# Performance work log

Measured on AMD Instinct MI355X. Metric: run time of the kernel, lower is better.

The kernel has to match this reference:

```python
import jax, jax.numpy as jnp
import numpy as np

B, C, H, W = 128, 2048, 14, 14
K = 112          # num_concepts
NUM_CLASSES = 200


def setup_inputs() -> dict:
    key = jax.random.key(0)
    ks = jax.random.split(key, 8)
    x = jax.random.normal(ks[0], (B, C, H, W), dtype=jnp.float32)
    concepts = jax.random.normal(ks[1], (K, C), dtype=jnp.float32)
    modulation = jax.random.normal(ks[2], (1, C), dtype=jnp.float32)
    background = jax.random.normal(ks[3], (1, C), dtype=jnp.float32)
    # concept_fc: Linear(C, 1)
    w_cfc = jax.random.normal(ks[4], (1, C), dtype=jnp.float32) / np.sqrt(C)
    b_cfc = jnp.zeros((1,), dtype=jnp.float32)
    # label_fc: Linear(C*K, num_classes)
    w_lfc = jax.random.normal(ks[5], (NUM_CLASSES, C * K), dtype=jnp.float32) / np.sqrt(C * K)
    b_lfc = jnp.zeros((NUM_CLASSES,), dtype=jnp.float32)
    return {"x": x, "concepts": concepts, "modulation": modulation,
            "background": background, "w_cfc": w_cfc, "b_cfc": b_cfc,
            "w_lfc": w_lfc, "b_lfc": b_lfc}


def reference(x, concepts, modulation, background, w_cfc, b_cfc, w_lfc, b_lfc):
    b, c, h, w = x.shape
    n = h * w
    x_flat = x.reshape(b, c, n).transpose(0, 2, 1)          # [b, n, c]
    cpts_wbg = jnp.concatenate([concepts, background], 0)   # [k+1, c]

    # cdist p=2 via ||a||^2 + ||x||^2 - 2 a.x
    a_sq = jnp.sum(cpts_wbg * cpts_wbg, -1)                 # [k+1]
    x_sq = jnp.sum(x_flat * x_flat, -1)                     # [b, n]
    dots = jnp.einsum('kc,bnc->bkn', cpts_wbg, x_flat)      # [b, k+1, n]
    d2 = a_sq[None, :, None] + x_sq[:, None, :] - 2.0 * dots
    dists = jnp.sqrt(jnp.maximum(d2, 0.0))                  # [b, k+1, n]

    attn = jax.nn.softmax(-dists, axis=1)                   # softmax over concepts
    cpt_score_maps = attn.reshape(b, -1, h, w)              # [b, k+1, h, w]

    cpt_reprs = jnp.einsum('bkn,bnc->bkc', attn[:, :-1, :], x_flat)  # [b, k, c]
    cpt_logits = jax.nn.sigmoid(
        jnp.einsum('bkc,oc->bko', cpt_reprs, w_cfc) + b_cfc).squeeze(-1)  # [b, k]

    g = cpt_logits[..., None]                               # [b, k, 1]
    cpts_mixed = g * concepts[None] + (1.0 - g) * modulation[None]  # [b, k, c]
    label_logits = cpts_mixed.reshape(b, -1) @ w_lfc.T + b_lfc      # [b, classes]

    return cpt_score_maps, cpt_logits, label_logits
```

## Files before the change

### kernel.cpp

```cpp
#include <hip/hip_runtime.h>
#include <hip/hip_bf16.h>
#include <math.h>

#define B 128
#define C 2048
#define N 196
#define K 112
#define KB 113
#define MROWS 128
#define XWROW 113
#define NCLS 200
#define CKC (C * K)
#define NT 13
#define MAIN_BLKS 416
#define PQ_BLKS 5600

#define OUT1_OFF 2834944
#define OUT2_OFF 2849280

typedef __attribute__((ext_vector_type(8))) short bf16x8;
typedef __attribute__((ext_vector_type(4))) float f32x4;

__device__ inline unsigned cvtpk(float a, float b) {
    union { __hip_bfloat162 h; unsigned u; } c;
    c.h.x = __float2bfloat16(a);
    c.h.y = __float2bfloat16(b);
    return c.u;
}
__device__ inline const float* row_src(int row, const float* concepts,
                                       const float* background, const float* wcfc) {
    if (row < K) return concepts + (size_t)row * C;
    if (row == K) return background;
    if (row == XWROW) return wcfc;
    return nullptr;
}
__device__ __forceinline__ void gl16(const void* g, void* l) {
    __builtin_amdgcn_global_load_lds(
        (const __attribute__((address_space(1))) unsigned*)g,
        (__attribute__((address_space(3))) unsigned*)l, 16, 0, 0);
}

__global__ __launch_bounds__(256)
void asq_kernel(const float* __restrict__ concepts, const float* __restrict__ background,
                const float* __restrict__ wcfc, float* __restrict__ asq) {
    const int row = blockIdx.x;
    const int tid = threadIdx.x;
    const float* src = row_src(row, concepts, background, wcfc);
    float local = 0.f;
    if (src) for (int i = tid; i < C; i += 256) { float v = src[i]; local += v * v; }
    for (int off = 32; off; off >>= 1) local += __shfl_down(local, off);
    __shared__ float red[4];
    if ((tid & 63) == 0) red[tid >> 6] = local;
    __syncthreads();
    if (tid == 0) asq[row] = red[0] + red[1] + red[2] + red[3];
}

__global__ __launch_bounds__(64)
void pack_kernel(const float* __restrict__ concepts, const float* __restrict__ background,
                 const float* __restrict__ wcfc, unsigned short* __restrict__ Afrag) {
    const int f = blockIdx.x;
    const int it = blockIdx.y;
    const int l = threadIdx.x;
    const int row = 16 * f + (l & 15);
    const int kb = 32 * it + 8 * (l >> 4);
    const float* src = row_src(row, concepts, background, wcfc);
    unsigned o[4] = {0u, 0u, 0u, 0u};
    if (src) {
        const float4 f0 = *reinterpret_cast<const float4*>(src + kb);
        const float4 f1 = *reinterpret_cast<const float4*>(src + kb + 4);
        o[0] = cvtpk(f0.x, f0.y); o[1] = cvtpk(f0.z, f0.w);
        o[2] = cvtpk(f1.x, f1.y); o[3] = cvtpk(f1.z, f1.w);
    }
    *reinterpret_cast<uint4*>(Afrag + (((size_t)it * 8 + f) * 64 + l) * 8) =
        make_uint4(o[0], o[1], o[2], o[3]);
}

__global__ __launch_bounds__(256, 2)
void fused_kernel(const float* __restrict__ x,
                  const unsigned short* __restrict__ Afrag,
                  const float* __restrict__ asq_g,
                  float* __restrict__ out0,
                  float* __restrict__ lpart,
                  const float* __restrict__ wlfc,
                  const float* __restrict__ concepts,
                  const float* __restrict__ modulation,
                  float* __restrict__ Rm, float* __restrict__ Qs) {
    __shared__ __align__(16) char smem[65536];
    const int tid = threadIdx.x;
    const int lane = tid & 63;
    const int w = tid >> 6;
    const int blkid = blockIdx.x;

    if (blkid < MAIN_BLKS) {
        const int gw = blkid * 4 + w;
        const int b = gw / NT;
        const int nt = gw - b * NT;
        const int n0 = nt * 16;
        const int lo = lane & 15, hi = lane >> 4;

        char* Abase = smem;
        char* Xw = smem + 32768 + w * 8192;

        const char* agl = (const char*)Afrag + w * 1024 + lane * 16;
        const int xr = lane >> 2, xc = lane & 3;
        const bool bad = (nt == NT - 1) && (xc != 0);
        const float* xlane = bad ? x
            : x + (size_t)b * C * N + (size_t)xr * N + (n0 + xc * 4);
        const char* xgl = (const char*)xlane;

        f32x4 acc[8];
#pragma unroll
        for (int f = 0; f < 8; ++f) acc[f] = (f32x4){0.f, 0.f, 0.f, 0.f};
        float xs = 0.f;

#define STAGE(SBUF) do {                                                        \
        gl16(agl,        Abase + (SBUF) * 8192 + 0 * 4096 + w * 1024);          \
        gl16(agl + 4096, Abase + (SBUF) * 8192 + 1 * 4096 + w * 1024);          \
        gl16(xgl,                  Xw + (SBUF) * 2048);                         \
        gl16(xgl + 16 * N * 4,     Xw + (SBUF) * 2048 + 1024);                  \
        agl += 8192; xgl += (size_t)32 * N * 4;                                 \
    } while (0)

#define PIPE_WAIT(NSTR) do {                                                    \
        asm volatile("s_waitcnt vmcnt(" NSTR ")" ::: "memory");                 \
        __builtin_amdgcn_sched_barrier(0);                                      \
        __builtin_amdgcn_s_barrier();                                           \
        asm volatile("" ::: "memory");                                          \
        __builtin_amdgcn_sched_barrier(0);                                      \
    } while (0)

#define CONS(BUF) do {                                                          \
        bf16x8 af[8];                                                           \
        _Pragma("unroll")                                                       \
        for (int f = 0; f < 8; ++f)                                             \
            af[f] = *reinterpret_cast<const bf16x8*>(                           \
                Abase + (BUF) * 8192 + f * 1024 + (lane << 4));                 \
        float xv[8];                                                            \
        _Pragma("unroll")                                                       \
        for (int j = 0; j < 8; ++j)                                             \
            xv[j] = *reinterpret_cast<const float*>(                            \
                Xw + (BUF) * 2048 + ((hi * 8 + j) << 6) + (lo << 2));           \
        union { unsigned u[4]; bf16x8 v; } bu;                                  \
        _Pragma("unroll")                                                       \
        for (int p = 0; p < 4; ++p) bu.u[p] = cvtpk(xv[2 * p], xv[2 * p + 1]); \
        _Pragma("unroll")                                                       \
        for (int j = 0; j < 8; ++j) xs += xv[j] * xv[j];                        \
        _Pragma("unroll")                                                       \
        for (int f = 0; f < 8; ++f)                                             \
            acc[f] = __builtin_amdgcn_mfma_f32_16x16x32_bf16(                   \
                af[f], bu.v, acc[f], 0, 0, 0);                                  \
    } while (0)

        STAGE(0); STAGE(1);
        for (int trip = 0; trip < 15; ++trip) {
            STAGE(2); PIPE_WAIT("8"); CONS(0);
            STAGE(3); PIPE_WAIT("8"); CONS(1);
            STAGE(0); PIPE_WAIT("8"); CONS(2);
            STAGE(1); PIPE_WAIT("8"); CONS(3);
        }
        STAGE(2); PIPE_WAIT("8"); CONS(0);
        STAGE(3); PIPE_WAIT("8"); CONS(1);
        PIPE_WAIT("4"); CONS(2);
        PIPE_WAIT("0"); CONS(3);

        float xsq = xs + __shfl_xor(xs, 16);
        xsq += __shfl_xor(xsq, 32);
        const float xw = __shfl(acc[7][1], lo);
        const int colg = n0 + lo;
        const bool colv = colg < N;

        float m = -3.4e38f;
#pragma unroll
        for (int f = 0; f < 8; ++f)
#pragma unroll
            for (int rr = 0; rr < 4; ++rr) {
                const int r = 16 * f + 4 * hi + rr;
                const bool valid = (f < 7) | ((hi == 0) & (rr == 0));
                if (valid) {
                    const float d2 = asq_g[r] + xsq - 2.f * acc[f][rr];
                    const float L = -sqrtf(fmaxf(d2, 0.f));
                    acc[f][rr] = L;
                    m = fmaxf(m, L);
                }
            }
        float M = fmaxf(m, __shfl_xor(m, 16));
        M = fmaxf(M, __shfl_xor(M, 32));
        float s = 0.f;
#pragma unroll
        for (int f = 0; f < 8; ++f)
#pragma unroll
            for (int rr = 0; rr < 4; ++rr) {
                const bool valid = (f < 7) | ((hi == 0) & (rr == 0));
                const float e = valid ? __expf(acc[f][rr] - M) : 0.f;
                acc[f][rr] = e;
                s += e;
            }
        float S = s + __shfl_xor(s, 16);
        S += __shfl_xor(S, 32);
        const float invS = 1.f / S;

        float* o0 = out0 + (size_t)b * KB * N + colg;
#pragma unroll
        for (int f = 0; f < 8; ++f)
#pragma unroll
            for (int rr = 0; rr < 4; ++rr) {
                const int r = 16 * f + 4 * hi + rr;
                const bool valid = (f < 7) | ((hi == 0) & (rr == 0));
                if (valid && colv) o0[(size_t)r * N] = acc[f][rr] * invS;
            }
#pragma unroll
        for (int f = 0; f < 7; ++f)
#pragma unroll
            for (int rr = 0; rr < 4; ++rr) {
                float pv = colv ? acc[f][rr] * invS * xw : 0.f;
                pv += __shfl_xor(pv, 1);
                pv += __shfl_xor(pv, 2);
                pv += __shfl_xor(pv, 4);
                pv += __shfl_xor(pv, 8);
                if (lo == 0)
                    lpart[((size_t)b * NT + nt) * K + 16 * f + 4 * hi + rr] = pv;
            }
    } else {
        const int wid = (blkid - MAIN_BLKS) * 4 + w;
        const int o = wid / K;
        const int k = wid % K;
        const float4* wp = reinterpret_cast<const float4*>(wlfc + (size_t)o * CKC + (size_t)k * C);
        const float4* cp = reinterpret_cast<const float4*>(concepts + (size_t)k * C);
        const float4* mp = reinterpret_cast<const float4*>(modulation);
        float s1 = 0.f, s2 = 0.f;
#pragma unroll
        for (int it = 0; it < 8; ++it) {
            const int idx = it * 64 + lane;
            const float4 w4 = wp[idx];
            const float4 c4 = cp[idx];
            const float4 m4 = mp[idx];
            s1 += w4.x * c4.x + w4.y * c4.y + w4.z * c4.z + w4.w * c4.w;
            s2 += w4.x * m4.x + w4.y * m4.y + w4.z * m4.z + w4.w * m4.w;
        }
        for (int off = 32; off; off >>= 1) {
            s1 += __shfl_down(s1, off);
            s2 += __shfl_down(s2, off);
        }
        if (lane == 0) { Rm[wid] = s1 - s2; Qs[wid] = s2; }
    }
}

__global__ __launch_bounds__(256)
void final_kernel(const float* __restrict__ lpart, const float* __restrict__ bcfc,
                  const float* __restrict__ Rm, const float* __restrict__ Qs,
                  const float* __restrict__ blfc,
                  float* __restrict__ out1, float* __restrict__ out2) {
    const int b = blockIdx.x;
    const int tid = threadIdx.x;
    __shared__ float g_s[K];
    if (tid < K) {
        const float* lp = lpart + (size_t)b * NT * K + tid;
        float v = bcfc[0];
#pragma unroll
        for (int t = 0; t < NT; ++t) v += lp[(size_t)t * K];
        const float g = 1.f / (1.f + __expf(-v));
        out1[b * K + tid] = g;
        g_s[tid] = g;
    }
    __syncthreads();
    if (tid < NCLS) {
        float acc = blfc[tid];
        const float* rp = Rm + (size_t)tid * K;
        const float* qp = Qs + (size_t)tid * K;
        for (int k = 0; k < K; ++k) acc = fmaf(g_s[k], rp[k], acc) + qp[k];
        out2[b * NCLS + tid] = acc;
    }
}

extern "C" void kernel_launch(void* const* d_in, const int* in_sizes, int n_in,
                              void* d_out, int out_size, void* d_ws, size_t ws_size,
                              hipStream_t stream) {
    const float* x          = (const float*)d_in[0];
    const float* concepts   = (const float*)d_in[1];
    const float* modulation = (const float*)d_in[2];
    const float* background = (const float*)d_in[3];
    const float* wcfc       = (const float*)d_in[4];
    const float* bcfc       = (const float*)d_in[5];
    const float* wlfc       = (const float*)d_in[6];
    const float* blfc       = (const float*)d_in[7];

    float* out  = (float*)d_out;
    float* out0 = out;
    float* out1 = out + OUT1_OFF;
    float* out2 = out + OUT2_OFF;

    float* ws    = (float*)d_ws;
    float* asq   = ws;
    float* lpart = asq + MROWS;
    float* Rm    = lpart + (size_t)B * NT * K;
    float* Qs    = Rm + NCLS * K;
    unsigned short* Afrag = (unsigned short*)(Qs + NCLS * K);

    asq_kernel<<<MROWS, 256, 0, stream>>>(concepts, background, wcfc, asq);
    pack_kernel<<<dim3(8, 64), 64, 0, stream>>>(concepts, background, wcfc, Afrag);
    fused_kernel<<<MAIN_BLKS + PQ_BLKS, 256, 0, stream>>>(
        x, Afrag, asq, out0, lpart, wlfc, concepts, modulation, Rm, Qs);
    final_kernel<<<B, 256, 0, stream>>>(lpart, bcfc, Rm, Qs, blfc, out1, out2);
}
```

Measured before the change: 112.0 us.

## Use single-wave blocks with 32-column tiles and triple-buffered A staging

Restructures the fused kernel to launch 64-thread blocks, each handling a 32-column slice of one batch with two MFMA accumulators per A fragment. The A-fragment loads are reused across both column halves, and block-wide barriers disappear because each block is a single wave. The pipeline becomes three-stage and the PQ section loops over four dot products per wave. The change cuts barrier cost and raises reuse of A. In exchange, each wave now loads the full A tile itself, because it can no longer be shared across four waves, and it holds more registers for the doubled accumulators.

Result: slower. 129.1 us (+15.2%).

```diff
diff --git a/kernel.cpp b/kernel.cpp
--- a/kernel.cpp
+++ b/kernel.cpp
@@ -11,8 +11,8 @@
 #define XWROW 113
 #define NCLS 200
 #define CKC (C * K)
-#define NT 13
-#define MAIN_BLKS 416
+#define NT 7
+#define MAIN_BLKS 896
 #define PQ_BLKS 5600
 
 #define OUT1_OFF 2834944
@@ -75,7 +75,7 @@
         make_uint4(o[0], o[1], o[2], o[3]);
 }
 
-__global__ __launch_bounds__(256, 2)
+__global__ __launch_bounds__(64)
 void fused_kernel(const float* __restrict__ x,
                   const unsigned short* __restrict__ Afrag,
                   const float* __restrict__ asq_g,
@@ -85,91 +85,101 @@
                   const float* __restrict__ concepts,
                   const float* __restrict__ modulation,
                   float* __restrict__ Rm, float* __restrict__ Qs) {
-    __shared__ __align__(16) char smem[65536];
-    const int tid = threadIdx.x;
-    const int lane = tid & 63;
-    const int w = tid >> 6;
+    __shared__ __align__(16) char smem[36864];
+    const int lane = threadIdx.x;
     const int blkid = blockIdx.x;
 
     if (blkid < MAIN_BLKS) {
-        const int gw = blkid * 4 + w;
-        const int b = gw / NT;
-        const int nt = gw - b * NT;
-        const int n0 = nt * 16;
+        const int b = blkid / NT;
+        const int nt = blkid - b * NT;
+        const int n0 = nt * 32;
         const int lo = lane & 15, hi = lane >> 4;
 
         char* Abase = smem;
-        char* Xw = smem + 32768 + w * 8192;
-
-        const char* agl = (const char*)Afrag + w * 1024 + lane * 16;
-        const int xr = lane >> 2, xc = lane & 3;
-        const bool bad = (nt == NT - 1) && (xc != 0);
-        const float* xlane = bad ? x
-            : x + (size_t)b * C * N + (size_t)xr * N + (n0 + xc * 4);
-        const char* xgl = (const char*)xlane;
-
-        f32x4 acc[8];
-#pragma unroll
-        for (int f = 0; f < 8; ++f) acc[f] = (f32x4){0.f, 0.f, 0.f, 0.f};
-        float xs = 0.f;
-
-#define STAGE(SBUF) do {                                                        \
-        gl16(agl,        Abase + (SBUF) * 8192 + 0 * 4096 + w * 1024);          \
-        gl16(agl + 4096, Abase + (SBUF) * 8192 + 1 * 4096 + w * 1024);          \
-        gl16(xgl,                  Xw + (SBUF) * 2048);                         \
-        gl16(xgl + 16 * N * 4,     Xw + (SBUF) * 2048 + 1024);                  \
+        char* Xbase = smem + 24576;
+
+        const char* agl = (const char*)Afrag + lane * 16;
+        const int segb_raw = n0 * 4 + (lane & 7) * 16;
+        const int segb = segb_raw < (N - 4) * 4 ? segb_raw : (N - 4) * 4;
+        const char* xgl = (const char*)x
+            + ((size_t)b * C + (lane >> 3)) * N * 4 + segb;
+
+        f32x4 acc[8][2];
+#pragma unroll
+        for (int f = 0; f < 8; ++f) {
+            acc[f][0] = (f32x4){0.f, 0.f, 0.f, 0.f};
+            acc[f][1] = (f32x4){0.f, 0.f, 0.f, 0.f};
+        }
+        float xs0 = 0.f, xs1 = 0.f;
+
+#define STAGE(BUF) do {                                                         \
+        _Pragma("unroll")                                                       \
+        for (int i_ = 0; i_ < 8; ++i_)                                          \
+            gl16(agl + i_ * 1024, Abase + (BUF) * 8192 + i_ * 1024);            \
+        _Pragma("unroll")                                                       \
+        for (int i_ = 0; i_ < 4; ++i_)                                          \
+            gl16(xgl + (size_t)i_ * 8 * N * 4, Xbase + (BUF) * 4096 + i_ * 1024);\
         agl += 8192; xgl += (size_t)32 * N * 4;                                 \
     } while (0)
 
 #define PIPE_WAIT(NSTR) do {                                                    \
         asm volatile("s_waitcnt vmcnt(" NSTR ")" ::: "memory");                 \
         __builtin_amdgcn_sched_barrier(0);                                      \
-        __builtin_amdgcn_s_barrier();                                           \
-        asm volatile("" ::: "memory");                                          \
-        __builtin_amdgcn_sched_barrier(0);                                      \
     } while (0)
 
 #define CONS(BUF) do {                                                          \
         bf16x8 af[8];                                                           \
         _Pragma("unroll")                                                       \
-        for (int f = 0; f < 8; ++f)                                             \
-            af[f] = *reinterpret_cast<const bf16x8*>(                           \
-                Abase + (BUF) * 8192 + f * 1024 + (lane << 4));                 \
-        float xv[8];                                                            \
-        _Pragma("unroll")                                                       \
-        for (int j = 0; j < 8; ++j)                                             \
-            xv[j] = *reinterpret_cast<const float*>(                            \
-                Xw + (BUF) * 2048 + ((hi * 8 + j) << 6) + (lo << 2));           \
-        union { unsigned u[4]; bf16x8 v; } bu;                                  \
-        _Pragma("unroll")                                                       \
-        for (int p = 0; p < 4; ++p) bu.u[p] = cvtpk(xv[2 * p], xv[2 * p + 1]); \
-        _Pragma("unroll")                                                       \
-        for (int j = 0; j < 8; ++j) xs += xv[j] * xv[j];                        \
-        _Pragma("unroll")                                                       \
-        for (int f = 0; f < 8; ++f)                                             \
-            acc[f] = __builtin_amdgcn_mfma_f32_16x16x32_bf16(                   \
-                af[f], bu.v, acc[f], 0, 0, 0);                                  \
+        for (int f_ = 0; f_ < 8; ++f_)                                          \
+            af[f_] = *reinterpret_cast<const bf16x8*>(                          \
+                Abase + (BUF) * 8192 + f_ * 1024 + (lane << 4));                \
+        float xv0[8], xv1[8];                                                   \
+        _Pragma("unroll")                                                       \
+        for (int j_ = 0; j_ < 8; ++j_) {                                        \
+            xv0[j_] = *reinterpret_cast<const float*>(                          \
+                Xbase + (BUF) * 4096 + ((hi * 8 + j_) << 7) + (lo << 2));       \
+            xv1[j_] = *reinterpret_cast<const float*>(                          \
+                Xbase + (BUF) * 4096 + ((hi * 8 + j_) << 7) + ((16 + lo) << 2));\
+        }                                                                       \
+        union { unsigned u[4]; bf16x8 v; } b0_, b1_;                            \
+        _Pragma("unroll")                                                       \
+        for (int p_ = 0; p_ < 4; ++p_) {                                        \
+            b0_.u[p_] = cvtpk(xv0[2 * p_], xv0[2 * p_ + 1]);                    \
+            b1_.u[p_] = cvtpk(xv1[2 * p_], xv1[2 * p_ + 1]);                    \
+        }                                                                       \
+        _Pragma("unroll")                                                       \
+        for (int j_ = 0; j_ < 8; ++j_) {                                        \
+            xs0 += xv0[j_] * xv0[j_];                                           \
+            xs1 += xv1[j_] * xv1[j_];                                           \
+        }                                                                       \
+        _Pragma("unroll")                                                       \
+        for (int f_ = 0; f_ < 8; ++f_) {                                        \
+            acc[f_][0] = __builtin_amdgcn_mfma_f32_16x16x32_bf16(               \
+                af[f_], b0_.v, acc[f_][0], 0, 0, 0);                            \
+            acc[f_][1] = __builtin_amdgcn_mfma_f32_16x16x32_bf16(               \
+                af[f_], b1_.v, acc[f_][1], 0, 0, 0);                            \
+        }                                                                       \
     } while (0)
 
         STAGE(0); STAGE(1);
-        for (int trip = 0; trip < 15; ++trip) {
-            STAGE(2); PIPE_WAIT("8"); CONS(0);
-            STAGE(3); PIPE_WAIT("8"); CONS(1);
-            STAGE(0); PIPE_WAIT("8"); CONS(2);
-            STAGE(1); PIPE_WAIT("8"); CONS(3);
+        for (int tp = 0; tp < 20; ++tp) {
+            PIPE_WAIT("12"); STAGE(2); CONS(0);
+            PIPE_WAIT("12"); STAGE(0); CONS(1);
+            PIPE_WAIT("12"); STAGE(1); CONS(2);
         }
-        STAGE(2); PIPE_WAIT("8"); CONS(0);
-        STAGE(3); PIPE_WAIT("8"); CONS(1);
-        PIPE_WAIT("4"); CONS(2);
-        PIPE_WAIT("0"); CONS(3);
-
-        float xsq = xs + __shfl_xor(xs, 16);
-        xsq += __shfl_xor(xsq, 32);
-        const float xw = __shfl(acc[7][1], lo);
-        const int colg = n0 + lo;
-        const bool colv = colg < N;
-
-        float m = -3.4e38f;
+        PIPE_WAIT("12"); STAGE(2); CONS(0);
+        PIPE_WAIT("12"); STAGE(0); CONS(1);
+        PIPE_WAIT("12"); CONS(2);
+        PIPE_WAIT("0");  CONS(0);
+
+        float xsq0 = xs0 + __shfl_xor(xs0, 16); xsq0 += __shfl_xor(xsq0, 32);
+        float xsq1 = xs1 + __shfl_xor(xs1, 16); xsq1 += __shfl_xor(xsq1, 32);
+        const float xw0 = __shfl(acc[7][0][1], lo);
+        const float xw1 = __shfl(acc[7][1][1], lo);
+        const bool cv0 = (n0 + lo) < N;
+        const bool cv1 = (n0 + 16 + lo) < N;
+
+        float m0 = -3.4e38f, m1 = -3.4e38f;
 #pragma unroll
         for (int f = 0; f < 8; ++f)
 #pragma unroll
@@ -177,42 +187,46 @@
                 const int r = 16 * f + 4 * hi + rr;
                 const bool valid = (f < 7) | ((hi == 0) & (rr == 0));
                 if (valid) {
-                    const float d2 = asq_g[r] + xsq - 2.f * acc[f][rr];
-                    const float L = -sqrtf(fmaxf(d2, 0.f));
-                    acc[f][rr] = L;
-                    m = fmaxf(m, L);
+                    const float aq = asq_g[r];
+                    float L0 = -sqrtf(fmaxf(aq + xsq0 - 2.f * acc[f][0][rr], 0.f));
+                    float L1 = -sqrtf(fmaxf(aq + xsq1 - 2.f * acc[f][1][rr], 0.f));
+                    acc[f][0][rr] = L0; acc[f][1][rr] = L1;
+                    m0 = fmaxf(m0, L0); m1 = fmaxf(m1, L1);
                 }
             }
-        float M = fmaxf(m, __shfl_xor(m, 16));
-        M = fmaxf(M, __shfl_xor(M, 32));
-        float s = 0.f;
+        float M0 = fmaxf(m0, __shfl_xor(m0, 16)); M0 = fmaxf(M0, __shfl_xor(M0, 32));
+        float M1 = fmaxf(m1, __shfl_xor(m1, 16)); M1 = fmaxf(M1, __shfl_xor(M1, 32));
+        float s0 = 0.f, s1 = 0.f;
 #pragma unroll
         for (int f = 0; f < 8; ++f)
 #pragma unroll
             for (int rr = 0; rr < 4; ++rr) {
                 const bool valid = (f < 7) | ((hi == 0) & (rr == 0));
-                const float e = valid ? __expf(acc[f][rr] - M) : 0.f;
-                acc[f][rr] = e;
-                s += e;
-            }
-        float S = s + __shfl_xor(s, 16);
-        S += __shfl_xor(S, 32);
-        const float invS = 1.f / S;
-
-        float* o0 = out0 + (size_t)b * KB * N + colg;
+                const float e0 = valid ? __expf(acc[f][0][rr] - M0) : 0.f;
+                const float e1 = valid ? __expf(acc[f][1][rr] - M1) : 0.f;
+                acc[f][0][rr] = e0; acc[f][1][rr] = e1;
+                s0 += e0; s1 += e1;
+            }
+        float S0 = s0 + __shfl_xor(s0, 16); S0 += __shfl_xor(S0, 32);
+        float S1 = s1 + __shfl_xor(s1, 16); S1 += __shfl_xor(S1, 32);
+        const float iv0 = 1.f / S0, iv1 = 1.f / S1;
+
+        float* o0 = out0 + (size_t)b * KB * N + n0 + lo;
 #pragma unroll
         for (int f = 0; f < 8; ++f)
 #pragma unroll
             for (int rr = 0; rr < 4; ++rr) {
                 const int r = 16 * f + 4 * hi + rr;
                 const bool valid = (f < 7) | ((hi == 0) & (rr == 0));
-                if (valid && colv) o0[(size_t)r * N] = acc[f][rr] * invS;
+                if (valid && cv0) o0[(size_t)r * N] = acc[f][0][rr] * iv0;
+                if (valid && cv1) o0[(size_t)r * N + 16] = acc[f][1][rr] * iv1;
             }
 #pragma unroll
         for (int f = 0; f < 7; ++f)
 #pragma unroll
             for (int rr = 0; rr < 4; ++rr) {
-                float pv = colv ? acc[f][rr] * invS * xw : 0.f;
+                float pv = (cv0 ? acc[f][0][rr] * iv0 * xw0 : 0.f)
+                         + (cv1 ? acc[f][1][rr] * iv1 * xw1 : 0.f);
                 pv += __shfl_xor(pv, 1);
                 pv += __shfl_xor(pv, 2);
                 pv += __shfl_xor(pv, 4);
@@ -221,27 +235,31 @@
                     lpart[((size_t)b * NT + nt) * K + 16 * f + 4 * hi + rr] = pv;
             }
     } else {
-        const int wid = (blkid - MAIN_BLKS) * 4 + w;
-        const int o = wid / K;
-        const int k = wid % K;
-        const float4* wp = reinterpret_cast<const float4*>(wlfc + (size_t)o * CKC + (size_t)k * C);
-        const float4* cp = reinterpret_cast<const float4*>(concepts + (size_t)k * C);
-        const float4* mp = reinterpret_cast<const float4*>(modulation);
-        float s1 = 0.f, s2 = 0.f;
-#pragma unroll
-        for (int it = 0; it < 8; ++it) {
-            const int idx = it * 64 + lane;
-            const float4 w4 = wp[idx];
-            const float4 c4 = cp[idx];
-            const float4 m4 = mp[idx];
-            s1 += w4.x * c4.x + w4.y * c4.y + w4.z * c4.z + w4.w * c4.w;
-            s2 += w4.x * m4.x + w4.y * m4.y + w4.z * m4.z + w4.w * m4.w;
+        const int wb = (blkid - MAIN_BLKS) * 4;
+#pragma unroll
+        for (int q = 0; q < 4; ++q) {
+            const int wid = wb + q;
+            const int o = wid / K;
+            const int k = wid % K;
+            const float4* wp = reinterpret_cast<const float4*>(wlfc + (size_t)o * CKC + (size_t)k * C);
+            const float4* cp = reinterpret_cast<const float4*>(concepts + (size_t)k * C);
+            const float4* mp = reinterpret_cast<const float4*>(modulation);
+            float s1 = 0.f, s2 = 0.f;
+#pragma unroll
+            for (int it = 0; it < 8; ++it) {
+                const int idx = it * 64 + lane;
+                const float4 w4 = wp[idx];
+                const float4 c4 = cp[idx];
+                const float4 m4 = mp[idx];
+                s1 += w4.x * c4.x + w4.y * c4.y + w4.z * c4.z + w4.w * c4.w;
+                s2 += w4.x * m4.x + w4.y * m4.y + w4.z * m4.z + w4.w * m4.w;
+            }
+            for (int off = 32; off; off >>= 1) {
+                s1 += __shfl_down(s1, off);
+                s2 += __shfl_down(s2, off);
+            }
+            if (lane == 0) { Rm[wid] = s1 - s2; Qs[wid] = s2; }
         }
-        for (int off = 32; off; off >>= 1) {
-            s1 += __shfl_down(s1, off);
-            s2 += __shfl_down(s2, off);
-        }
-        if (lane == 0) { Rm[wid] = s1 - s2; Qs[wid] = s2; }
     }
 }
 
@@ -298,7 +316,7 @@
 
     asq_kernel<<<MROWS, 256, 0, stream>>>(concepts, background, wcfc, asq);
     pack_kernel<<<dim3(8, 64), 64, 0, stream>>>(concepts, background, wcfc, Afrag);
-    fused_kernel<<<MAIN_BLKS + PQ_BLKS, 256, 0, stream>>>(
+    fused_kernel<<<MAIN_BLKS + PQ_BLKS, 64, 0, stream>>>(
         x, Afrag, asq, out0, lpart, wlfc, concepts, modulation, Rm, Qs);
     final_kernel<<<B, 256, 0, stream>>>(lpart, bcfc, Rm, Qs, blfc, out1, out2);
 }
```

## Process one whole image per 512-thread block with an LDS-transposed bf16 X tile

Applied to the files above, without the earlier changes.

The main GEMM is restructured so each block owns a full image (all 196 spatial columns) and each of its 8 waves owns one 16-row concept fragment. X chunks are loaded contiguously into LDS, converted to bf16 and transposed in a separate pass, then reused across 13 column tiles, so each A fragment is loaded once per image instead of once per 16-column tile. The softmax max and sum now need cross-wave reductions through LDS, and the per-tile lpart partials disappear. The pipeline is shallower, with a double-buffered A, a single-buffered X and several barriers per step, and the grid shrinks to 128 main blocks, which may leave the GPU underfilled.

Result: slower. 121.3 us (+8.2%).

```diff
diff --git a/kernel.cpp b/kernel.cpp
--- a/kernel.cpp
+++ b/kernel.cpp
@@ -11,9 +11,10 @@
 #define XWROW 113
 #define NCLS 200
 #define CKC (C * K)
-#define NT 13
-#define MAIN_BLKS 416
-#define PQ_BLKS 5600
+#define MAIN_BLKS 128
+#define PQ_BLKS 700
+#define XSTEP 25088
+#define IMGB (C * N * 4)
 
 #define OUT1_OFF 2834944
 #define OUT2_OFF 2849280
@@ -38,6 +39,11 @@
     __builtin_amdgcn_global_load_lds(
         (const __attribute__((address_space(1))) unsigned*)g,
         (__attribute__((address_space(3))) unsigned*)l, 16, 0, 0);
+}
+__device__ __forceinline__ void gl4(const void* g, void* l) {
+    __builtin_amdgcn_global_load_lds(
+        (const __attribute__((address_space(1))) unsigned*)g,
+        (__attribute__((address_space(3))) unsigned*)l, 4, 0, 0);
 }
 
 __global__ __launch_bounds__(256)
@@ -59,10 +65,10 @@
 void pack_kernel(const float* __restrict__ concepts, const float* __restrict__ background,
                  const float* __restrict__ wcfc, unsigned short* __restrict__ Afrag) {
     const int f = blockIdx.x;
-    const int it = blockIdx.y;
+    const int kwg = blockIdx.y;
     const int l = threadIdx.x;
     const int row = 16 * f + (l & 15);
-    const int kb = 32 * it + 8 * (l >> 4);
+    const int kb = 32 * kwg + 8 * (l >> 4);
     const float* src = row_src(row, concepts, background, wcfc);
     unsigned o[4] = {0u, 0u, 0u, 0u};
     if (src) {
@@ -71,11 +77,11 @@
         o[0] = cvtpk(f0.x, f0.y); o[1] = cvtpk(f0.z, f0.w);
         o[2] = cvtpk(f1.x, f1.y); o[3] = cvtpk(f1.z, f1.w);
     }
-    *reinterpret_cast<uint4*>(Afrag + (((size_t)it * 8 + f) * 64 + l) * 8) =
+    *reinterpret_cast<uint4*>(Afrag + (((size_t)kwg * 8 + f) * 64 + l) * 8) =
         make_uint4(o[0], o[1], o[2], o[3]);
 }
 
-__global__ __launch_bounds__(256, 2)
+__global__ __launch_bounds__(512)
 void fused_kernel(const float* __restrict__ x,
                   const unsigned short* __restrict__ Afrag,
                   const float* __restrict__ asq_g,
@@ -85,163 +91,236 @@
                   const float* __restrict__ concepts,
                   const float* __restrict__ modulation,
                   float* __restrict__ Rm, float* __restrict__ Qs) {
-    __shared__ __align__(16) char smem[65536];
+    __shared__ __align__(16) char smem[61952];
     const int tid = threadIdx.x;
     const int lane = tid & 63;
     const int w = tid >> 6;
     const int blkid = blockIdx.x;
 
     if (blkid < MAIN_BLKS) {
-        const int gw = blkid * 4 + w;
-        const int b = gw / NT;
-        const int nt = gw - b * NT;
-        const int n0 = nt * 16;
+        const int b = blkid;
+        float* Xf = (float*)smem;
+        char* Ab0 = smem + 25600;
+        unsigned short* XT = (unsigned short*)(smem + 41984);
+        float* xsqL = (float*)(smem + 58624);
+        float* pmw = (float*)smem;
+        float* xwL = (float*)(smem + 8192);
+
         const int lo = lane & 15, hi = lane >> 4;
-
-        char* Abase = smem;
-        char* Xw = smem + 32768 + w * 8192;
-
-        const char* agl = (const char*)Afrag + w * 1024 + lane * 16;
-        const int xr = lane >> 2, xc = lane & 3;
-        const bool bad = (nt == NT - 1) && (xc != 0);
-        const float* xlane = bad ? x
-            : x + (size_t)b * C * N + (size_t)xr * N + (n0 + xc * 4);
-        const char* xgl = (const char*)xlane;
-
-        f32x4 acc[8];
-#pragma unroll
-        for (int f = 0; f < 8; ++f) acc[f] = (f32x4){0.f, 0.f, 0.f, 0.f};
+        const char* xim = (const char*)x + (size_t)b * IMGB;
+        const char* Ag = (const char*)Afrag;
+
+        const bool act = tid < 416;
+        const int h = (act && tid >= 208) ? 1 : 0;
+        const int cc = act ? (tid - 208 * h) : 0;
+
+        f32x4 acc[13];
+#pragma unroll
+        for (int ct = 0; ct < 13; ++ct) acc[ct] = (f32x4){0.f, 0.f, 0.f, 0.f};
         float xs = 0.f;
 
-#define STAGE(SBUF) do {                                                        \
-        gl16(agl,        Abase + (SBUF) * 8192 + 0 * 4096 + w * 1024);          \
-        gl16(agl + 4096, Abase + (SBUF) * 8192 + 1 * 4096 + w * 1024);          \
-        gl16(xgl,                  Xw + (SBUF) * 2048);                         \
-        gl16(xgl + 16 * N * 4,     Xw + (SBUF) * 2048 + 1024);                  \
-        agl += 8192; xgl += (size_t)32 * N * 4;                                 \
-    } while (0)
-
-#define PIPE_WAIT(NSTR) do {                                                    \
-        asm volatile("s_waitcnt vmcnt(" NSTR ")" ::: "memory");                 \
+#define ISSUE_X(JJ) do {                                                        \
+        const char* sx_ = xim + (size_t)(JJ) * XSTEP;                           \
+        gl16(sx_ + (3 * w + 0) * 1024 + lane * 16, smem + (3 * w + 0) * 1024);  \
+        gl16(sx_ + (3 * w + 1) * 1024 + lane * 16, smem + (3 * w + 1) * 1024);  \
+        gl16(sx_ + (3 * w + 2) * 1024 + lane * 16, smem + (3 * w + 2) * 1024);  \
+        if (w < 2) gl4(sx_ + 24576 + w * 256 + lane * 4,                        \
+                       smem + 24576 + w * 256);                                 \
+    } while (0)
+
+#define ISSUE_A(JJ) do {                                                        \
+        gl16(Ag + (size_t)(JJ) * 8192 + w * 1024 + lane * 16,                   \
+             Ab0 + ((JJ) & 1) * 8192 + w * 1024);                               \
+    } while (0)
+
+#define VM0() do {                                                              \
+        asm volatile("s_waitcnt vmcnt(0)" ::: "memory");                        \
         __builtin_amdgcn_sched_barrier(0);                                      \
+    } while (0)
+
+#define LBAR() do {                                                             \
+        asm volatile("s_waitcnt lgkmcnt(0)" ::: "memory");                      \
         __builtin_amdgcn_s_barrier();                                           \
-        asm volatile("" ::: "memory");                                          \
         __builtin_amdgcn_sched_barrier(0);                                      \
     } while (0)
 
-#define CONS(BUF) do {                                                          \
-        bf16x8 af[8];                                                           \
+#define CONVERT() do {                                                          \
+        if (act) {                                                              \
+            const float* xp_ = Xf + (16 * h) * 196 + cc;                        \
+            float v_[16];                                                       \
+            _Pragma("unroll")                                                   \
+            for (int q_ = 0; q_ < 16; ++q_) v_[q_] = xp_[q_ * 196];             \
+            _Pragma("unroll")                                                   \
+            for (int q_ = 0; q_ < 16; ++q_) xs += v_[q_] * v_[q_];              \
+            unsigned u_[8];                                                     \
+            _Pragma("unroll")                                                   \
+            for (int p_ = 0; p_ < 8; ++p_)                                      \
+                u_[p_] = cvtpk(v_[2 * p_], v_[2 * p_ + 1]);                     \
+            unsigned short* xt_ = XT + cc * 40 + h * 16;                        \
+            *reinterpret_cast<uint4*>(xt_) = make_uint4(u_[0], u_[1], u_[2], u_[3]); \
+            *reinterpret_cast<uint4*>(xt_ + 8) = make_uint4(u_[4], u_[5], u_[6], u_[7]); \
+        }                                                                       \
+    } while (0)
+
+#define MFMA_STEP(JJ) do {                                                      \
+        const char* Ab_ = Ab0 + ((JJ) & 1) * 8192;                              \
+        const bf16x8 afr_ = *reinterpret_cast<const bf16x8*>(                   \
+            Ab_ + ((w * 64 + lane) << 4));                                      \
         _Pragma("unroll")                                                       \
-        for (int f = 0; f < 8; ++f)                                             \
-            af[f] = *reinterpret_cast<const bf16x8*>(                           \
-                Abase + (BUF) * 8192 + f * 1024 + (lane << 4));                 \
-        float xv[8];                                                            \
-        _Pragma("unroll")                                                       \
-        for (int j = 0; j < 8; ++j)                                             \
-            xv[j] = *reinterpret_cast<const float*>(                            \
-                Xw + (BUF) * 2048 + ((hi * 8 + j) << 6) + (lo << 2));           \
-        union { unsigned u[4]; bf16x8 v; } bu;                                  \
-        _Pragma("unroll")                                                       \
-        for (int p = 0; p < 4; ++p) bu.u[p] = cvtpk(xv[2 * p], xv[2 * p + 1]); \
-        _Pragma("unroll")                                                       \
-        for (int j = 0; j < 8; ++j) xs += xv[j] * xv[j];                        \
-        _Pragma("unroll")                                                       \
-        for (int f = 0; f < 8; ++f)                                             \
-            acc[f] = __builtin_amdgcn_mfma_f32_16x16x32_bf16(                   \
-                af[f], bu.v, acc[f], 0, 0, 0);                                  \
-    } while (0)
-
-        STAGE(0); STAGE(1);
-        for (int trip = 0; trip < 15; ++trip) {
-            STAGE(2); PIPE_WAIT("8"); CONS(0);
-            STAGE(3); PIPE_WAIT("8"); CONS(1);
-            STAGE(0); PIPE_WAIT("8"); CONS(2);
-            STAGE(1); PIPE_WAIT("8"); CONS(3);
-        }
-        STAGE(2); PIPE_WAIT("8"); CONS(0);
-        STAGE(3); PIPE_WAIT("8"); CONS(1);
-        PIPE_WAIT("4"); CONS(2);
-        PIPE_WAIT("0"); CONS(3);
-
-        float xsq = xs + __shfl_xor(xs, 16);
-        xsq += __shfl_xor(xsq, 32);
-        const float xw = __shfl(acc[7][1], lo);
-        const int colg = n0 + lo;
-        const bool colv = colg < N;
-
-        float m = -3.4e38f;
-#pragma unroll
-        for (int f = 0; f < 8; ++f)
+        for (int ct_ = 0; ct_ < 13; ++ct_) {                                    \
+            const bf16x8 bfr_ = *reinterpret_cast<const bf16x8*>(               \
+                (const char*)XT + (ct_ * 16 + lo) * 80 + hi * 16);              \
+            acc[ct_] = __builtin_amdgcn_mfma_f32_16x16x32_bf16(                 \
+                afr_, bfr_, acc[ct_], 0, 0, 0);                                 \
+        }                                                                       \
+    } while (0)
+
+        ISSUE_X(0); ISSUE_A(0);
+#pragma unroll 1
+        for (int j = 0; j < 63; ++j) {
+            VM0(); LBAR();
+            CONVERT();
+            LBAR();
+            ISSUE_X(j + 1);
+            MFMA_STEP(j);
+            ISSUE_A(j + 1);
+        }
+        VM0(); LBAR(); CONVERT(); LBAR(); MFMA_STEP(63);
+
+        __syncthreads();
+        if (act) xsqL[h * 208 + cc] = xs;
+        if (w == 7 && hi == 0) {
+#pragma unroll
+            for (int ct = 0; ct < 13; ++ct) xwL[ct * 16 + lo] = acc[ct][1];
+        }
+        __syncthreads();
+
+        float xq[13];
+#pragma unroll
+        for (int ct = 0; ct < 13; ++ct) {
+            const int c = ct * 16 + lo;
+            xq[ct] = xsqL[c] + xsqL[208 + c];
+        }
+        float aq[4];
+#pragma unroll
+        for (int rr = 0; rr < 4; ++rr) aq[rr] = asq_g[16 * w + 4 * hi + rr];
+        const bool v4 = (w < 7);
+
+        float mct[13];
+#pragma unroll
+        for (int ct = 0; ct < 13; ++ct) {
 #pragma unroll
             for (int rr = 0; rr < 4; ++rr) {
-                const int r = 16 * f + 4 * hi + rr;
-                const bool valid = (f < 7) | ((hi == 0) & (rr == 0));
-                if (valid) {
-                    const float d2 = asq_g[r] + xsq - 2.f * acc[f][rr];
-                    const float L = -sqrtf(fmaxf(d2, 0.f));
-                    acc[f][rr] = L;
-                    m = fmaxf(m, L);
+                const float d2 = aq[rr] + xq[ct] - 2.f * acc[ct][rr];
+                acc[ct][rr] = -sqrtf(fmaxf(d2, 0.f));
+            }
+            float mv = -3.4e38f;
+            if (v4) mv = fmaxf(fmaxf(acc[ct][0], acc[ct][1]),
+                               fmaxf(acc[ct][2], acc[ct][3]));
+            else if (hi == 0) mv = acc[ct][0];
+            mv = fmaxf(mv, __shfl_xor(mv, 16));
+            mv = fmaxf(mv, __shfl_xor(mv, 32));
+            mct[ct] = mv;
+        }
+        if (hi == 0) {
+#pragma unroll
+            for (int ct = 0; ct < 13; ++ct) pmw[w * 208 + ct * 16 + lo] = mct[ct];
+        }
+        __syncthreads();
+        float Mct[13];
+#pragma unroll
+        for (int ct = 0; ct < 13; ++ct) {
+            float mm = -3.4e38f;
+#pragma unroll
+            for (int ww = 0; ww < 8; ++ww)
+                mm = fmaxf(mm, pmw[ww * 208 + ct * 16 + lo]);
+            Mct[ct] = mm;
+        }
+        __syncthreads();
+        float sct[13];
+#pragma unroll
+        for (int ct = 0; ct < 13; ++ct) {
+            float ss = 0.f;
+#pragma unroll
+            for (int rr = 0; rr < 4; ++rr) {
+                const bool valid = v4 || (hi == 0 && rr == 0);
+                const float e = valid ? __expf(acc[ct][rr] - Mct[ct]) : 0.f;
+                acc[ct][rr] = e;
+                ss += e;
+            }
+            ss += __shfl_xor(ss, 16);
+            ss += __shfl_xor(ss, 32);
+            sct[ct] = ss;
+        }
+        if (hi == 0) {
+#pragma unroll
+            for (int ct = 0; ct < 13; ++ct) pmw[w * 208 + ct * 16 + lo] = sct[ct];
+        }
+        __syncthreads();
+        float inv[13];
+#pragma unroll
+        for (int ct = 0; ct < 13; ++ct) {
+            float SS = 0.f;
+#pragma unroll
+            for (int ww = 0; ww < 8; ++ww) SS += pmw[ww * 208 + ct * 16 + lo];
+            inv[ct] = 1.f / SS;
+        }
+
+        float* o0 = out0 + (size_t)b * KB * N;
+#pragma unroll
+        for (int ct = 0; ct < 13; ++ct) {
+            const int c = ct * 16 + lo;
+            const bool cv = c < N;
+#pragma unroll
+            for (int rr = 0; rr < 4; ++rr) {
+                const int r = 16 * w + 4 * hi + rr;
+                const bool valid = v4 || (hi == 0 && rr == 0);
+                if (valid && cv) o0[(size_t)r * N + c] = acc[ct][rr] * inv[ct];
+            }
+        }
+        if (v4) {
+#pragma unroll
+            for (int rr = 0; rr < 4; ++rr) {
+                float pv = 0.f;
+#pragma unroll
+                for (int ct = 0; ct < 13; ++ct) {
+                    const int c = ct * 16 + lo;
+                    const float term = acc[ct][rr] * inv[ct] * xwL[c];
+                    pv += (c < N) ? term : 0.f;
                 }
-            }
-        float M = fmaxf(m, __shfl_xor(m, 16));
-        M = fmaxf(M, __shfl_xor(M, 32));
-        float s = 0.f;
-#pragma unroll
-        for (int f = 0; f < 8; ++f)
-#pragma unroll
-            for (int rr = 0; rr < 4; ++rr) {
-                const bool valid = (f < 7) | ((hi == 0) & (rr == 0));
-                const float e = valid ? __expf(acc[f][rr] - M) : 0.f;
-                acc[f][rr] = e;
-                s += e;
-            }
-        float S = s + __shfl_xor(s, 16);
-        S += __shfl_xor(S, 32);
-        const float invS = 1.f / S;
-
-        float* o0 = out0 + (size_t)b * KB * N + colg;
-#pragma unroll
-        for (int f = 0; f < 8; ++f)
-#pragma unroll
-            for (int rr = 0; rr < 4; ++rr) {
-                const int r = 16 * f + 4 * hi + rr;
-                const bool valid = (f < 7) | ((hi == 0) & (rr == 0));
-                if (valid && colv) o0[(size_t)r * N] = acc[f][rr] * invS;
-            }
-#pragma unroll
-        for (int f = 0; f < 7; ++f)
-#pragma unroll
-            for (int rr = 0; rr < 4; ++rr) {
-                float pv = colv ? acc[f][rr] * invS * xw : 0.f;
                 pv += __shfl_xor(pv, 1);
                 pv += __shfl_xor(pv, 2);
                 pv += __shfl_xor(pv, 4);
                 pv += __shfl_xor(pv, 8);
-                if (lo == 0)
-                    lpart[((size_t)b * NT + nt) * K + 16 * f + 4 * hi + rr] = pv;
-            }
+                if (lo == 0) lpart[(size_t)b * K + 16 * w + 4 * hi + rr] = pv;
+            }
+        }
     } else {
-        const int wid = (blkid - MAIN_BLKS) * 4 + w;
-        const int o = wid / K;
-        const int k = wid % K;
-        const float4* wp = reinterpret_cast<const float4*>(wlfc + (size_t)o * CKC + (size_t)k * C);
-        const float4* cp = reinterpret_cast<const float4*>(concepts + (size_t)k * C);
-        const float4* mp = reinterpret_cast<const float4*>(modulation);
-        float s1 = 0.f, s2 = 0.f;
-#pragma unroll
-        for (int it = 0; it < 8; ++it) {
-            const int idx = it * 64 + lane;
-            const float4 w4 = wp[idx];
-            const float4 c4 = cp[idx];
-            const float4 m4 = mp[idx];
-            s1 += w4.x * c4.x + w4.y * c4.y + w4.z * c4.z + w4.w * c4.w;
-            s2 += w4.x * m4.x + w4.y * m4.y + w4.z * m4.z + w4.w * m4.w;
-        }
-        for (int off = 32; off; off >>= 1) {
-            s1 += __shfl_down(s1, off);
-            s2 += __shfl_down(s2, off);
-        }
-        if (lane == 0) { Rm[wid] = s1 - s2; Qs[wid] = s2; }
+        const int wb = (blkid - MAIN_BLKS) * 32 + w * 4;
+#pragma unroll
+        for (int q = 0; q < 4; ++q) {
+            const int wid = wb + q;
+            const int o = wid / K;
+            const int k = wid % K;
+            const float4* wp = reinterpret_cast<const float4*>(wlfc + (size_t)o * CKC + (size_t)k * C);
+            const float4* cp = reinterpret_cast<const float4*>(concepts + (size_t)k * C);
+            const float4* mp = reinterpret_cast<const float4*>(modulation);
+            float s1 = 0.f, s2 = 0.f;
+#pragma unroll
+            for (int it = 0; it < 8; ++it) {
+                const int idx = it * 64 + lane;
+                const float4 w4 = wp[idx];
+                const float4 c4 = cp[idx];
+                const float4 m4 = mp[idx];
+                s1 += w4.x * c4.x + w4.y * c4.y + w4.z * c4.z + w4.w * c4.w;
+                s2 += w4.x * m4.x + w4.y * m4.y + w4.z * m4.z + w4.w * m4.w;
+            }
+            for (int off = 32; off; off >>= 1) {
+                s1 += __shfl_down(s1, off);
+                s2 += __shfl_down(s2, off);
+            }
+            if (lane == 0) { Rm[wid] = s1 - s2; Qs[wid] = s2; }
+        }
     }
 }
 
@@ -254,10 +333,7 @@
     const int tid = threadIdx.x;
     __shared__ float g_s[K];
     if (tid < K) {
-        const float* lp = lpart + (size_t)b * NT * K + tid;
-        float v = bcfc[0];
-#pragma unroll
-        for (int t = 0; t < NT; ++t) v += lp[(size_t)t * K];
+        const float v = lpart[(size_t)b * K + tid] + bcfc[0];
         const float g = 1.f / (1.f + __expf(-v));
         out1[b * K + tid] = g;
         g_s[tid] = g;
@@ -292,13 +368,13 @@
     float* ws    = (float*)d_ws;
     float* asq   = ws;
     float* lpart = asq + MROWS;
-    float* Rm    = lpart + (size_t)B * NT * K;
+    float* Rm    = lpart + (size_t)B * K;
     float* Qs    = Rm + NCLS * K;
     unsigned short* Afrag = (unsigned short*)(Qs + NCLS * K);
 
     asq_kernel<<<MROWS, 256, 0, stream>>>(concepts, background, wcfc, asq);
     pack_kernel<<<dim3(8, 64), 64, 0, stream>>>(concepts, background, wcfc, Afrag);
-    fused_kernel<<<MAIN_BLKS + PQ_BLKS, 256, 0, stream>>>(
+    fused_kernel<<<MAIN_BLKS + PQ_BLKS, 512, 0, stream>>>(
         x, Afrag, asq, out0, lpart, wlfc, concepts, modulation, Rm, Qs);
     final_kernel<<<B, 256, 0, stream>>>(lpart, bcfc, Rm, Qs, blfc, out1, out2);
 }
```
